# Kernel tuning notes

Measured on AMD Instinct MI355X. Metric: run time of the kernel, lower is better.

The kernel has to match this reference:

```python
import jax, jax.numpy as jnp
import numpy as np


def setup_inputs() -> dict:
    key = jax.random.key(0)
    k1, k2, k3, k4 = jax.random.split(key, 4)
    B_, n, u, da = 32, 2048, 1024, 512
    H = jax.random.normal(k1, (B_, n, u), dtype=jnp.float32)
    # glorot-style scaling for params
    W = jax.random.normal(k2, (u, da), dtype=jnp.float32) * (2.0 / (u + da)) ** 0.5
    Bb = jax.random.normal(k3, (1, da), dtype=jnp.float32) * (2.0 / (1 + da)) ** 0.5
    U = jax.random.normal(k4, (da, 1), dtype=jnp.float32) * (2.0 / (da + 1)) ** 0.5
    return {"H": H, "W": W, "B": Bb, "U": U}


def reference(H, W, B, U):
    # V = tanh(H @ W + B)           [batch, n, da]
    V = jnp.tanh(jnp.einsum("bnu,ud->bnd", H, W) + B[None, :, :])
    # scores = V @ U, softmax over sequence axis (axis=1)   [batch, n, 1]
    scores = jnp.einsum("bnd,do->bno", V, U)
    VU = jax.nn.softmax(scores, axis=1)
    # elementwise weighting of the original input
    Ma = H * VU
    return (Ma, VU)
```

## Files before the change

kernel.cpp:

```cpp
#include <hip/hip_runtime.h>
#include <hip/hip_bf16.h>

typedef __attribute__((ext_vector_type(8))) __bf16 bf16x8;
typedef __attribute__((ext_vector_type(4))) float f32x4;

#define N_SEQ   2048
#define N_BATCH 32
#define DIM_U   1024
#define NROWS   65536
#define MA_ELEMS ((size_t)NROWS * DIM_U)

__device__ __forceinline__ float tanh_fast(float x) {
    x = fminf(fmaxf(x, -15.f), 15.f);
    float e = __expf(2.f * x);
    return (e - 1.f) * __builtin_amdgcn_rcpf(e + 1.f);
}

__global__ void wpack_kernel(const float* __restrict__ W, __bf16* __restrict__ Wp) {
    int F   = blockIdx.x * 256 + threadIdx.x;
    int col = F & 255;
    int g   = (F >> 8) & 3;
    int nh  = (F >> 10) & 1;
    int it  = F >> 11;
    int k0  = it * 32 + g * 8;
    int c   = nh * 256 + col;
    bf16x8 o;
#pragma unroll
    for (int j = 0; j < 8; ++j) o[j] = (__bf16)W[(k0 + j) * 512 + c];
    *reinterpret_cast<bf16x8*>(Wp + (size_t)F * 8) = o;
}

__global__ __launch_bounds__(512, 4) void score_gemm_kernel(
    const float* __restrict__ H, const __bf16* __restrict__ Wp,
    const float* __restrict__ Bb, const float* __restrict__ Uv,
    float* __restrict__ sp)
{
    __shared__ __align__(16) char lds[49152];
    const int tid  = threadIdx.x;
    const int lane = tid & 63;
    const int wid  = tid >> 6;
    const int c15  = lane & 15;
    const int hi   = lane >> 4;
    const int wr   = wid >> 2;
    const int wc   = wid & 3;

    const int bid = blockIdx.x;
    const int L   = (bid & 7) * 128 + (bid >> 3);
    const int mt = L >> 1, nh = L & 1;
    const long rowbase = (long)mt * 128;

    const int arow = tid >> 2, ag = tid & 3;
    const float* aglob = H + (rowbase + arow) * DIM_U + ag * 8;
    const int awoff = ag * 2048 + ((arow ^ ag) * 16);

    const int abase0 = hi * 2048 + (wr * 64 + (c15 ^ hi)) * 16;
    const int bbase0 = 16384 + hi * 4096 + (wc * 64 + c15) * 16;

#define GLD(srcp, dstoff)                                                      \
    __builtin_amdgcn_global_load_lds(                                          \
        (const __attribute__((address_space(1))) void*)(const void*)(srcp),    \
        (__attribute__((address_space(3))) void*)(void*)(lds + (dstoff)), 16, 0, 0)

#define STAGE_B(it_, db_) {                                                    \
        const __bf16* bg_ = Wp + (((size_t)(it_) * 2 + nh) * 1024) * 8;        \
        GLD(bg_ + (size_t)tid * 8,         16384 + (db_) * 16384 + tid * 16);  \
        GLD(bg_ + ((size_t)tid + 512) * 8, 16384 + (db_) * 16384 + 8192 + tid * 16); }

#define LOADA(La_, Lb_, it_) {                                                 \
        const float* p_ = aglob + (it_) * 32;                                  \
        La_ = *reinterpret_cast<const f32x4*>(p_);                             \
        Lb_ = *reinterpret_cast<const f32x4*>(p_ + 4); }

#define CVTW(La_, Lb_, db_) {                                                  \
        bf16x8 pk_ = {(__bf16)La_.x, (__bf16)La_.y, (__bf16)La_.z,             \
                      (__bf16)La_.w, (__bf16)Lb_.x, (__bf16)Lb_.y,             \
                      (__bf16)Lb_.z, (__bf16)Lb_.w};                           \
        *reinterpret_cast<bf16x8*>(lds + (db_) * 8192 + awoff) = pk_; }

#define COMPUTE(db_) {                                                         \
        bf16x8 af[4], bf[4];                                                   \
        _Pragma("unroll")                                                      \
        for (int m = 0; m < 4; ++m)                                            \
            af[m] = *reinterpret_cast<const bf16x8*>(                          \
                lds + (db_) * 8192 + abase0 + m * 256);                        \
        _Pragma("unroll")                                                      \
        for (int n = 0; n < 4; ++n)                                            \
            bf[n] = *reinterpret_cast<const bf16x8*>(                          \
                lds + (db_) * 16384 + bbase0 + n * 256);                       \
        __builtin_amdgcn_s_setprio(1);                                         \
        _Pragma("unroll")                                                      \
        for (int m = 0; m < 4; ++m) {                                          \
            _Pragma("unroll")                                                  \
            for (int n = 0; n < 4; ++n)                                        \
                acc[m][n] = __builtin_amdgcn_mfma_f32_16x16x32_bf16(           \
                    af[m], bf[n], acc[m][n], 0, 0, 0);                         \
        }                                                                      \
        __builtin_amdgcn_s_setprio(0); }

#define WAITBAR2 { asm volatile("s_waitcnt vmcnt(2) lgkmcnt(0)" ::: "memory"); \
                   __builtin_amdgcn_s_barrier(); }
#define WAITBAR0 { asm volatile("s_waitcnt vmcnt(0) lgkmcnt(0)" ::: "memory"); \
                   __builtin_amdgcn_s_barrier(); }

    f32x4 acc[4][4];
#pragma unroll
    for (int m = 0; m < 4; ++m)
#pragma unroll
        for (int n = 0; n < 4; ++n) acc[m][n] = f32x4{0.f, 0.f, 0.f, 0.f};

    f32x4 L0a, L0b, L1a, L1b;

    LOADA(L0a, L0b, 0);
    CVTW(L0a, L0b, 0);
    STAGE_B(0, 0);
    __builtin_amdgcn_sched_barrier(0);
    LOADA(L1a, L1b, 1);
    __builtin_amdgcn_sched_barrier(0);
    WAITBAR2;

    for (int tt = 0; tt < 15; ++tt) {
        const int t0 = 2 * tt;
        STAGE_B(t0 + 1, 1);
        __builtin_amdgcn_sched_barrier(0);
        LOADA(L0a, L0b, t0 + 2);
        __builtin_amdgcn_sched_barrier(0);
        COMPUTE(0);
        CVTW(L1a, L1b, 1);
        WAITBAR2;
        STAGE_B(t0 + 2, 0);
        __builtin_amdgcn_sched_barrier(0);
        LOADA(L1a, L1b, t0 + 3);
        __builtin_amdgcn_sched_barrier(0);
        COMPUTE(1);
        CVTW(L0a, L0b, 0);
        WAITBAR2;
    }
    STAGE_B(31, 1);
    COMPUTE(0);
    CVTW(L1a, L1b, 1);
    WAITBAR0;
    COMPUTE(1);

    float bias[4], uu[4];
#pragma unroll
    for (int n = 0; n < 4; ++n) {
        int col = nh * 256 + wc * 64 + n * 16 + c15;
        bias[n] = Bb[col];
        uu[n]   = Uv[col];
    }
    float* partial = reinterpret_cast<float*>(lds);
#pragma unroll
    for (int m = 0; m < 4; ++m) {
        float pr[4];
#pragma unroll
        for (int r = 0; r < 4; ++r) pr[r] = 0.f;
#pragma unroll
        for (int n = 0; n < 4; ++n)
#pragma unroll
            for (int r = 0; r < 4; ++r)
                pr[r] += tanh_fast(acc[m][n][r] + bias[n]) * uu[n];
#pragma unroll
        for (int r = 0; r < 4; ++r) {
            float v = pr[r];
            v += __shfl_xor(v, 1); v += __shfl_xor(v, 2);
            v += __shfl_xor(v, 4); v += __shfl_xor(v, 8);
            if (c15 == 0)
                partial[wc * 128 + wr * 64 + m * 16 + hi * 4 + r] = v;
        }
    }
    __syncthreads();
    if (tid < 128) {
        float sc = (partial[tid] + partial[128 + tid]) +
                   (partial[256 + tid] + partial[384 + tid]);
        sp[(size_t)nh * NROWS + rowbase + tid] = sc;
    }
}

__global__ void softmax_kernel(const float* __restrict__ sp, float* __restrict__ VU) {
    __shared__ float red[8];
    const int b = blockIdx.x, tid = threadIdx.x;
    const int lane = tid & 63, wid = tid >> 6;
    float v[8];
    float mx = -3.0e38f;
#pragma unroll
    for (int j = 0; j < 8; ++j) {
        int x = b * N_SEQ + tid + j * 256;
        v[j] = sp[x] + sp[NROWS + x];
        mx = fmaxf(mx, v[j]);
    }
#pragma unroll
    for (int off = 1; off < 64; off <<= 1) mx = fmaxf(mx, __shfl_xor(mx, off));
    if (lane == 0) red[wid] = mx;
    __syncthreads();
    mx = fmaxf(fmaxf(red[0], red[1]), fmaxf(red[2], red[3]));
    float e[8], sum = 0.f;
#pragma unroll
    for (int j = 0; j < 8; ++j) { e[j] = __expf(v[j] - mx); sum += e[j]; }
#pragma unroll
    for (int off = 1; off < 64; off <<= 1) sum += __shfl_xor(sum, off);
    if (lane == 0) red[4 + wid] = sum;
    __syncthreads();
    float total = (red[4] + red[5]) + (red[6] + red[7]);
    float rinv = 1.f / total;
#pragma unroll
    for (int j = 0; j < 8; ++j) VU[b * N_SEQ + tid + j * 256] = e[j] * rinv;
}

__global__ void ma_kernel(const float* __restrict__ H, const float* __restrict__ VU,
                          float* __restrict__ Ma) {
    const int stride = gridDim.x * blockDim.x;
    const int n4 = (int)(MA_ELEMS / 4);
    for (int i4 = blockIdx.x * blockDim.x + threadIdx.x; i4 < n4; i4 += stride) {
        float sc = VU[i4 >> 8];
        f32x4 h = reinterpret_cast<const f32x4*>(H)[i4];
        __builtin_nontemporal_store(h * sc, reinterpret_cast<f32x4*>(Ma) + i4);
    }
}

extern "C" void kernel_launch(void* const* d_in, const int* in_sizes, int n_in,
                              void* d_out, int out_size, void* d_ws, size_t ws_size,
                              hipStream_t stream) {
    const float* H  = (const float*)d_in[0];
    const float* W  = (const float*)d_in[1];
    const float* Bb = (const float*)d_in[2];
    const float* Uv = (const float*)d_in[3];

    float* out = (float*)d_out;
    float* Ma  = out;
    float* VU  = out + MA_ELEMS;
    float*  sp = out;
    __bf16* Wp = (__bf16*)(out + 131072);

    wpack_kernel<<<256, 256, 0, stream>>>(W, Wp);
    score_gemm_kernel<<<1024, 512, 0, stream>>>(H, Wp, Bb, Uv, sp);
    softmax_kernel<<<N_BATCH, 256, 0, stream>>>(sp, VU);
    ma_kernel<<<2048, 256, 0, stream>>>(H, VU, Ma);
}
```

Baseline: 168.4 us.

## Load packed W fragments directly into registers instead of staging through LDS

Replaces the global_load_lds staging of the pre-packed bf16 W tile with direct per-lane global loads into register fragments, double-buffered in registers. LDS shrinks from 48KB to 16KB, which may allow more resident blocks, and the B-side LDS reads and waits go away. The trade-off is that each wave now fetches its B fragments from global/L2 itself, so there are redundant loads across waves sharing columns, more register pressure, and exposed load latency now that the barrier no longer waits on vmcnt.

```diff
diff --git a/kernel.cpp b/kernel.cpp
--- a/kernel.cpp
+++ b/kernel.cpp
@@ -35,7 +35,7 @@
     const float* __restrict__ Bb, const float* __restrict__ Uv,
     float* __restrict__ sp)
 {
-    __shared__ __align__(16) char lds[49152];
+    __shared__ __align__(16) char lds[16384];
     const int tid  = threadIdx.x;
     const int lane = tid & 63;
     const int wid  = tid >> 6;
@@ -54,17 +54,14 @@
     const int awoff = ag * 2048 + ((arow ^ ag) * 16);
 
     const int abase0 = hi * 2048 + (wr * 64 + (c15 ^ hi)) * 16;
-    const int bbase0 = 16384 + hi * 4096 + (wc * 64 + c15) * 16;
-
-#define GLD(srcp, dstoff)                                                      \
-    __builtin_amdgcn_global_load_lds(                                          \
-        (const __attribute__((address_space(1))) void*)(const void*)(srcp),    \
-        (__attribute__((address_space(3))) void*)(void*)(lds + (dstoff)), 16, 0, 0)
-
-#define STAGE_B(it_, db_) {                                                    \
-        const __bf16* bg_ = Wp + (((size_t)(it_) * 2 + nh) * 1024) * 8;        \
-        GLD(bg_ + (size_t)tid * 8,         16384 + (db_) * 16384 + tid * 16);  \
-        GLD(bg_ + ((size_t)tid + 512) * 8, 16384 + (db_) * 16384 + 8192 + tid * 16); }
+
+    const bf16x8* wpb = reinterpret_cast<const bf16x8*>(Wp) +
+                        ((size_t)nh * 1024 + hi * 256 + wc * 64 + c15);
+
+#define LOADB(bf_, it_) {                                                      \
+        const bf16x8* bp_ = wpb + (size_t)(it_) * 2048;                        \
+        _Pragma("unroll")                                                      \
+        for (int n_ = 0; n_ < 4; ++n_) bf_[n_] = bp_[n_ * 16]; }
 
 #define LOADA(La_, Lb_, it_) {                                                 \
         const float* p_ = aglob + (it_) * 32;                                  \
@@ -77,30 +74,24 @@
                       (__bf16)Lb_.z, (__bf16)Lb_.w};                           \
         *reinterpret_cast<bf16x8*>(lds + (db_) * 8192 + awoff) = pk_; }
 
-#define COMPUTE(db_) {                                                         \
-        bf16x8 af[4], bf[4];                                                   \
+#define COMPUTE(db_, bf_) {                                                    \
+        bf16x8 af[4];                                                          \
         _Pragma("unroll")                                                      \
-        for (int m = 0; m < 4; ++m)                                            \
-            af[m] = *reinterpret_cast<const bf16x8*>(                          \
-                lds + (db_) * 8192 + abase0 + m * 256);                        \
-        _Pragma("unroll")                                                      \
-        for (int n = 0; n < 4; ++n)                                            \
-            bf[n] = *reinterpret_cast<const bf16x8*>(                          \
-                lds + (db_) * 16384 + bbase0 + n * 256);                       \
+        for (int m_ = 0; m_ < 4; ++m_)                                         \
+            af[m_] = *reinterpret_cast<const bf16x8*>(                         \
+                lds + (db_) * 8192 + abase0 + m_ * 256);                       \
         __builtin_amdgcn_s_setprio(1);                                         \
         _Pragma("unroll")                                                      \
-        for (int m = 0; m < 4; ++m) {                                          \
+        for (int m_ = 0; m_ < 4; ++m_) {                                       \
             _Pragma("unroll")                                                  \
-            for (int n = 0; n < 4; ++n)                                        \
-                acc[m][n] = __builtin_amdgcn_mfma_f32_16x16x32_bf16(           \
-                    af[m], bf[n], acc[m][n], 0, 0, 0);                         \
+            for (int n_ = 0; n_ < 4; ++n_)                                     \
+                acc[m_][n_] = __builtin_amdgcn_mfma_f32_16x16x32_bf16(         \
+                    af[m_], bf_[n_], acc[m_][n_], 0, 0, 0);                    \
         }                                                                      \
         __builtin_amdgcn_s_setprio(0); }
 
-#define WAITBAR2 { asm volatile("s_waitcnt vmcnt(2) lgkmcnt(0)" ::: "memory"); \
-                   __builtin_amdgcn_s_barrier(); }
-#define WAITBAR0 { asm volatile("s_waitcnt vmcnt(0) lgkmcnt(0)" ::: "memory"); \
-                   __builtin_amdgcn_s_barrier(); }
+#define BAR { asm volatile("s_waitcnt lgkmcnt(0)" ::: "memory");               \
+              __builtin_amdgcn_s_barrier(); }
 
     f32x4 acc[4][4];
 #pragma unroll
@@ -109,37 +100,36 @@
         for (int n = 0; n < 4; ++n) acc[m][n] = f32x4{0.f, 0.f, 0.f, 0.f};
 
     f32x4 L0a, L0b, L1a, L1b;
+    bf16x8 bfA[4], bfB[4];
 
     LOADA(L0a, L0b, 0);
     CVTW(L0a, L0b, 0);
-    STAGE_B(0, 0);
+    LOADB(bfA, 0);
     __builtin_amdgcn_sched_barrier(0);
     LOADA(L1a, L1b, 1);
     __builtin_amdgcn_sched_barrier(0);
-    WAITBAR2;
+    BAR;
 
     for (int tt = 0; tt < 15; ++tt) {
         const int t0 = 2 * tt;
-        STAGE_B(t0 + 1, 1);
-        __builtin_amdgcn_sched_barrier(0);
+        LOADB(bfB, t0 + 1);
         LOADA(L0a, L0b, t0 + 2);
         __builtin_amdgcn_sched_barrier(0);
-        COMPUTE(0);
+        COMPUTE(0, bfA);
         CVTW(L1a, L1b, 1);
-        WAITBAR2;
-        STAGE_B(t0 + 2, 0);
-        __builtin_amdgcn_sched_barrier(0);
+        BAR;
+        LOADB(bfA, t0 + 2);
         LOADA(L1a, L1b, t0 + 3);
         __builtin_amdgcn_sched_barrier(0);
-        COMPUTE(1);
+        COMPUTE(1, bfB);
         CVTW(L0a, L0b, 0);
-        WAITBAR2;
-    }
-    STAGE_B(31, 1);
-    COMPUTE(0);
+        BAR;
+    }
+    LOADB(bfB, 31);
+    COMPUTE(0, bfA);
     CVTW(L1a, L1b, 1);
-    WAITBAR0;
-    COMPUTE(1);
+    BAR;
+    COMPUTE(1, bfB);
 
     float bias[4], uu[4];
 #pragma unroll
```

After: 283.4 us. +68.3%, slower.
